# Performance work log

Measured on AMD Instinct MI355X. Metric: run time of the kernel, lower is better.

Reference implementation:

```python
import jax, jax.numpy as jnp
import numpy as np
import math

N_NODES = 20000
N_EDGES = 320000
MUL = 64          # multiplicity of each irrep block
N_BASIS = 10
N_HID = 100
W_NUMEL = 4 * MUL  # 4 'uvu' instructions, v=1


def setup_inputs() -> dict:
    key = jax.random.key(0)
    ks = jax.random.split(key, 16)
    node_input = jax.random.normal(ks[0], (N_NODES, 4 * MUL), dtype=jnp.float32)  # 64x0e + 64x1o -> 64 + 192
    node_attr = jnp.ones((N_NODES, 1), dtype=jnp.float32)
    node_deg = jax.random.randint(ks[1], (N_NODES, 1), 1, 33).astype(jnp.float32)
    edge_src = jax.random.randint(ks[2], (N_EDGES,), 0, N_NODES)
    edge_dst = jax.random.randint(ks[3], (N_EDGES,), 0, N_NODES)
    edge_attr = jax.random.normal(ks[4], (N_EDGES, 4), dtype=jnp.float32)  # sh: 1x0e + 1x1o
    edge_length_embedded = jax.random.uniform(ks[5], (N_EDGES, N_BASIS), dtype=jnp.float32)
    # FullyConnectedTensorProduct weights (node_attr is 1x0e -> per-irrep linear mixing)
    W_li0 = jax.random.normal(ks[6], (MUL, MUL), dtype=jnp.float32)
    W_li1 = jax.random.normal(ks[7], (MUL, MUL), dtype=jnp.float32)
    W_lm0 = jax.random.normal(ks[8], (MUL, MUL), dtype=jnp.float32)
    W_lm1 = jax.random.normal(ks[9], (MUL, MUL), dtype=jnp.float32)
    # radial MLP: number_of_basis -> radial_neurons -> weight_numel (no bias, e3nn FullyConnectedNet style)
    W_mlp1 = jax.random.normal(ks[10], (N_BASIS, N_HID), dtype=jnp.float32)
    W_mlp2 = jax.random.normal(ks[11], (N_HID, W_NUMEL), dtype=jnp.float32)
    # linear_output: irreps_mid (128x0e + 128x1o) x 1x0e -> 64x0e + 64x1o
    W_lo0 = jax.random.normal(ks[12], (2 * MUL, MUL), dtype=jnp.float32)
    W_lo1 = jax.random.normal(ks[13], (2 * MUL, MUL), dtype=jnp.float32)
    return dict(node_input=node_input, node_attr=node_attr, node_deg=node_deg,
                edge_attr=edge_attr, edge_length_embedded=edge_length_embedded,
                W_li0=W_li0, W_li1=W_li1, W_lm0=W_lm0, W_lm1=W_lm1,
                W_mlp1=W_mlp1, W_mlp2=W_mlp2, W_lo0=W_lo0, W_lo1=W_lo1,
                edge_src=edge_src, edge_dst=edge_dst)


def _split(x):
    # split 64x0e + 64x1o feature vector into scalar [*,64] and vector [*,64,3] parts
    s = x[..., :MUL]
    v = x[..., MUL:].reshape(x.shape[:-1] + (MUL, 3))
    return s, v


def _fctp(s, v, W0, W1, attr, fan_in):
    # FullyConnectedTensorProduct with 1x0e attr: per-irrep linear, path-normalized
    inv = 1.0 / math.sqrt(fan_in)
    o0 = jnp.einsum('nu,uk->nk', s, W0) * attr * inv
    o1 = jnp.einsum('num,uk->nkm', v, W1) * attr[..., None] * inv
    return o0, o1


def reference(node_input, node_attr, node_deg, edge_attr, edge_length_embedded,
              W_li0, W_li1, W_lm0, W_lm1, W_mlp1, W_mlp2, W_lo0, W_lo1,
              edge_src, edge_dst):
    N = node_input.shape[0]
    x0, x1 = _split(node_input)

    # linear_input then degree pre-normalization
    f0, f1 = _fctp(x0, x1, W_li0, W_li1, node_attr, MUL)
    deg_isqrt = 1.0 / jnp.sqrt(node_deg)            # [N,1]
    f0 = f0 * deg_isqrt
    f1 = f1 * deg_isqrt[..., None]

    # linear_mask (skip path)
    m0, m1 = _fctp(x0, x1, W_lm0, W_lm1, node_attr, MUL)

    # radial MLP -> per-edge tensor-product weights [E, 256]
    h = jax.nn.silu(edge_length_embedded @ W_mlp1 / math.sqrt(N_BASIS))
    ew = (h @ W_mlp2) / math.sqrt(N_HID)
    wa, wb, wc, wd = ew[:, :MUL], ew[:, MUL:2*MUL], ew[:, 2*MUL:3*MUL], ew[:, 3*MUL:]

    # gather source-node features per edge
    g0 = f0[edge_src]                                # [E,64]
    g1 = f1[edge_src]                                # [E,64,3]
    y0 = edge_attr[:, 0]                             # [E]   1x0e
    y1 = edge_attr[:, 1:4]                           # [E,3] 1x1o

    # 'uvu' tensor product paths (block-diagonal equivariant contractions)
    m0a = wa * g0 * y0[:, None]                                        # 0e x 0e -> 0e
    m0b = wb * jnp.einsum('eum,em->eu', g1, y1) / math.sqrt(3.0)       # 1o x 1o -> 0e
    m1a = wc[:, :, None] * g0[:, :, None] * y1[:, None, :]             # 0e x 1o -> 1o
    m1b = wd[:, :, None] * g1 * y0[:, None, None]                      # 1o x 0e -> 1o

    # scatter-sum into destination nodes (irreps_mid = 128x0e + 128x1o)
    s_mid = jax.ops.segment_sum(jnp.concatenate([m0a, m0b], axis=1), edge_dst, num_segments=N)          # [N,128]
    v_mid = jax.ops.segment_sum(jnp.concatenate([m1a, m1b], axis=1), edge_dst, num_segments=N)          # [N,128,3]

    # degree post-normalization
    s_mid = s_mid * deg_isqrt
    v_mid = v_mid * deg_isqrt[..., None]

    # linear_output
    o0, o1 = _fctp(s_mid, v_mid, W_lo0, W_lo1, node_attr, 2 * MUL)

    # masked skip combination; output_mask is all ones here (every out irrep is reachable)
    c_s, c_x = math.sin(math.pi / 8), math.cos(math.pi / 8)
    out0 = c_s * m0 + c_x * o0                       # [N,64]
    out1 = c_s * m1 + c_x * o1                       # [N,64,3]
    return jnp.concatenate([out0, out1.reshape(N, 3 * MUL)], axis=1)  # [N,256]
```

## Files before the change

### kernel.cpp

```cpp
#include <hip/hip_runtime.h>
#include <hip/hip_bf16.h>
#include <math.h>

#define N_NODES 20000
#define N_EDGES 320000

#define INV1   0.31622776601683794f
#define SC2    0.1f
#define IS3    0.5773502691896258f
#define C_S    0.3826834323650898f
#define C_X    0.9238795325112867f
#define INV64  0.125f
#define INVLO  0.08838834764831845f

typedef short     short8 __attribute__((ext_vector_type(8)));
typedef float     f32x4  __attribute__((ext_vector_type(4)));

__device__ __forceinline__ float silu_f(float x) {
    return x / (1.0f + expf(-x));
}
__device__ __forceinline__ unsigned short f2bf(float x) {
    __hip_bfloat16 h = __float2bfloat16(x);
    return *reinterpret_cast<unsigned short*>(&h);
}
__device__ __forceinline__ float bf2f(unsigned short u) {
    __hip_bfloat16 h;
    *reinterpret_cast<unsigned short*>(&h) = u;
    return __bfloat162float(h);
}

__global__ __launch_bounds__(256) void k_node_in(
    const float* __restrict__ ni, const float* __restrict__ attr,
    const float* __restrict__ deg,
    const float* __restrict__ Wli0, const float* __restrict__ Wli1,
    const float* __restrict__ Wlm0, const float* __restrict__ Wlm1,
    ushort4* __restrict__ fvb, float* __restrict__ out)
{
    __shared__ float raw[4][256];
    const int wave = threadIdx.x >> 6;
    const int lane = threadIdx.x & 63;
    const int n = blockIdx.x * 4 + wave;

    const float* row = ni + (size_t)n * 256;
    raw[wave][lane      ] = row[lane      ];
    raw[wave][lane + 64 ] = row[lane + 64 ];
    raw[wave][lane + 128] = row[lane + 128];
    raw[wave][lane + 192] = row[lane + 192];
    __syncthreads();

    float f0 = 0.f, m0 = 0.f;
    float f1x = 0.f, f1y = 0.f, f1z = 0.f;
    float m1x = 0.f, m1y = 0.f, m1z = 0.f;
    #pragma unroll 4
    for (int t = 0; t < 64; ++t) {
        float xs  = raw[wave][t];
        float xv0 = raw[wave][64 + t*3    ];
        float xv1 = raw[wave][64 + t*3 + 1];
        float xv2 = raw[wave][64 + t*3 + 2];
        float a0 = Wli0[t*64 + lane];
        float a1 = Wli1[t*64 + lane];
        float b0 = Wlm0[t*64 + lane];
        float b1 = Wlm1[t*64 + lane];
        f0  += xs  * a0;   m0  += xs  * b0;
        f1x += xv0 * a1;   f1y += xv1 * a1;   f1z += xv2 * a1;
        m1x += xv0 * b1;   m1y += xv1 * b1;   m1z += xv2 * b1;
    }

    const float a   = attr[n] * INV64;
    const float dis = 1.0f / sqrtf(deg[n]);
    const float fa  = a * dis;

    ushort4 pk;
    pk.x = f2bf(f0  * fa);
    pk.y = f2bf(f1x * fa);
    pk.z = f2bf(f1y * fa);
    pk.w = f2bf(f1z * fa);
    fvb[(size_t)n * 64 + lane] = pk;

    float* orow = out + (size_t)n * 256;
    orow[lane] = C_S * m0 * a;
    orow[64 + lane*3    ] = C_S * m1x * a;
    orow[64 + lane*3 + 1] = C_S * m1y * a;
    orow[64 + lane*3 + 2] = C_S * m1z * a;
}

__global__ __launch_bounds__(256) void k_w2t(
    const float* __restrict__ W2, const float* __restrict__ W1,
    unsigned short* __restrict__ w2t, unsigned short* __restrict__ w1t)
{
    const int i = blockIdx.x * 256 + threadIdx.x;
    if (i < 32768) {
        const int n = i >> 7, k = i & 127;
        w2t[i] = (k < 100) ? f2bf(W2[k*256 + n] * SC2) : (unsigned short)0;
    } else if (i < 32768 + 3584) {
        const int j = i - 32768;
        const int n = j >> 5, k = j & 31;
        w1t[j] = (k < 10 && n < 100) ? f2bf(W1[k*100 + n] * INV1)
                                     : (unsigned short)0;
    }
}

__global__ __launch_bounds__(256) void k_hist(const int* __restrict__ edst,
                                              int* __restrict__ hist) {
    const int e = blockIdx.x * 256 + threadIdx.x;
    if (e < N_EDGES) atomicAdd(&hist[edst[e]], 1);
}

__global__ __launch_bounds__(1024) void k_scan(const int* __restrict__ hist,
                                               int* __restrict__ starts,
                                               int* __restrict__ cursor) {
    __shared__ int part[1024];
    const int t = threadIdx.x;
    const int C = 20;
    const int base = t * C;
    int s = 0;
    for (int i = 0; i < C; ++i) {
        const int idx = base + i;
        if (idx < N_NODES) s += hist[idx];
    }
    part[t] = s;
    __syncthreads();
    for (int off = 1; off < 1024; off <<= 1) {
        int v = (t >= off) ? part[t - off] : 0;
        __syncthreads();
        part[t] += v;
        __syncthreads();
    }
    int run = part[t] - s;
    for (int i = 0; i < C; ++i) {
        const int idx = base + i;
        if (idx < N_NODES) {
            starts[idx] = run;
            cursor[idx] = run;
            run += hist[idx];
        }
    }
    if (t == 1023) starts[N_NODES] = N_EDGES;
}

__global__ __launch_bounds__(256) void k_scatter(
    const int* __restrict__ esrc, const int* __restrict__ edst,
    const float4* __restrict__ eattr4, const float* __restrict__ elen,
    int* __restrict__ cursor, int* __restrict__ esrc_s,
    float4* __restrict__ eattrs, unsigned short* __restrict__ elen_sb)
{
    const int e = blockIdx.x * 256 + threadIdx.x;
    if (e < N_EDGES) {
        const int p = atomicAdd(&cursor[edst[e]], 1);
        esrc_s[p] = esrc[e];
        eattrs[p] = eattr4[e];
        const float* el = elen + (size_t)e * 10;
        unsigned short v[32];
        #pragma unroll
        for (int b = 0; b < 10; ++b) v[b] = f2bf(el[b]);
        #pragma unroll
        for (int b = 10; b < 32; ++b) v[b] = 0;
        short8* dst = (short8*)(elen_sb + (size_t)p * 32);
        #pragma unroll
        for (int s = 0; s < 4; ++s) {
            short8 pk;
            #pragma unroll
            for (int j = 0; j < 8; ++j) pk[j] = (short)v[s*8 + j];
            dst[s] = pk;
        }
    }
}

__global__ __launch_bounds__(256, 4) void k_mlp(
    const unsigned short* __restrict__ elen_sb,
    const unsigned short* __restrict__ w1t,
    const unsigned short* __restrict__ w2t,
    unsigned short* __restrict__ ew)
{
    __shared__ unsigned short Hs[128 * 136];
    const int t    = threadIdx.x;
    const int w    = t >> 6;
    const int lane = t & 63;
    const int m15  = lane & 15;
    const int q    = lane >> 4;
    const int eb   = w * 32;
    const int e0   = blockIdx.x * 128;

    {
        const int r = eb + (lane >> 1);
        const int c = 112 + (lane & 1) * 8;
        short8 z = {0,0,0,0,0,0,0,0};
        *(short8*)&Hs[r*136 + c] = z;
    }

    short8 xa0 = *(const short8*)(elen_sb + (size_t)(e0 + eb      + m15)*32 + q*8);
    short8 xa1 = *(const short8*)(elen_sb + (size_t)(e0 + eb + 16 + m15)*32 + q*8);

    for (int nt = 0; nt < 7; ++nt) {
        short8 bw = *(const short8*)(w1t + (nt*16 + m15)*32 + q*8);
        f32x4 z4 = {0.f, 0.f, 0.f, 0.f};
        f32x4 h0 = __builtin_amdgcn_mfma_f32_16x16x32_bf16(xa0, bw, z4, 0, 0, 0);
        f32x4 h1 = __builtin_amdgcn_mfma_f32_16x16x32_bf16(xa1, bw, z4, 0, 0, 0);
        #pragma unroll
        for (int r = 0; r < 4; ++r) {
            Hs[(eb      + q*4 + r)*136 + nt*16 + m15] = f2bf(silu_f(h0[r]));
            Hs[(eb + 16 + q*4 + r)*136 + nt*16 + m15] = f2bf(silu_f(h1[r]));
        }
    }

    short8 A0[4], A1[4];
    #pragma unroll
    for (int s = 0; s < 4; ++s) {
        A0[s] = *(const short8*)&Hs[(eb      + m15)*136 + s*32 + q*8];
        A1[s] = *(const short8*)&Hs[(eb + 16 + m15)*136 + s*32 + q*8];
    }

    unsigned short* stg = &Hs[eb * 136];
    unsigned short* gb2 = ew + (size_t)(e0 + eb) * 256;
    #pragma unroll
    for (int half = 0; half < 2; ++half) {
        for (int nt8 = 0; nt8 < 8; ++nt8) {
            const int nt = half*8 + nt8;
            f32x4 c0 = {0.f,0.f,0.f,0.f}, c1 = {0.f,0.f,0.f,0.f};
            const unsigned short* bp = w2t + ((size_t)(nt*16 + m15) << 7);
            #pragma unroll
            for (int s = 0; s < 4; ++s) {
                short8 B = *(const short8*)(bp + s*32 + q*8);
                c0 = __builtin_amdgcn_mfma_f32_16x16x32_bf16(A0[s], B, c0, 0, 0, 0);
                c1 = __builtin_amdgcn_mfma_f32_16x16x32_bf16(A1[s], B, c1, 0, 0, 0);
            }
            #pragma unroll
            for (int r = 0; r < 4; ++r) {
                stg[(     q*4 + r)*136 + nt8*16 + m15] = f2bf(c0[r]);
                stg[(16 + q*4 + r)*136 + nt8*16 + m15] = f2bf(c1[r]);
            }
        }
        for (int r = 0; r < 32; ++r) {
            const unsigned int v =
                (unsigned int)stg[r*136 + lane] |
                ((unsigned int)stg[r*136 + 64 + lane] << 16);
            *(unsigned int*)(gb2 + (size_t)r*256 + lane*4 + half*2) = v;
        }
    }
}

__global__ __launch_bounds__(256) void k_gather(
    const int* __restrict__ starts, const int* __restrict__ esrc_s,
    const float4* __restrict__ eattrs, const unsigned short* __restrict__ ew,
    const ushort4* __restrict__ fvb,
    const float* __restrict__ attr, const float* __restrict__ deg,
    const float* __restrict__ Wlo0, const float* __restrict__ Wlo1,
    float* __restrict__ out)
{
    __shared__ float sm[4][512];
    const int wave = threadIdx.x >> 6;
    const int lane = threadIdx.x & 63;
    const int n = blockIdx.x * 4 + wave;

    const int beg = starts[n], end = starts[n + 1];
    float sA=0.f, sB=0.f;
    float vA0=0.f, vA1=0.f, vA2=0.f;
    float vB0=0.f, vB1=0.f, vB2=0.f;

    for (int base = beg; base < end; base += 64) {
        const int cnt = min(64, end - base);
        int    srcv = 0;
        float4 eav  = make_float4(0.f, 0.f, 0.f, 0.f);
        if (lane < cnt) {
            srcv = esrc_s[base + lane];
            eav  = eattrs[base + lane];
        }
        #pragma unroll 2
        for (int j = 0; j < cnt; ++j) {
            const int   src = __shfl(srcv, j);
            const float y0  = __shfl(eav.x, j);
            const float y10 = __shfl(eav.y, j);
            const float y11 = __shfl(eav.z, j);
            const float y12 = __shfl(eav.w, j);

            const ushort4 w4 = *(const ushort4*)(ew + (size_t)(base + j)*256 + lane*4);
            const float wa = bf2f(w4.x);
            const float wb = bf2f(w4.y);
            const float wc = bf2f(w4.z);
            const float wd = bf2f(w4.w);

            const ushort4 g4 = fvb[(size_t)src * 64 + lane];
            const float g0  = bf2f(g4.x);
            const float g10 = bf2f(g4.y);
            const float g11 = bf2f(g4.z);
            const float g12 = bf2f(g4.w);

            const float dotv = g10*y10 + g11*y11 + g12*y12;
            sA += wa * g0 * y0;
            sB += wb * dotv;
            const float t0 = wc * g0;
            vA0 += t0 * y10;  vA1 += t0 * y11;  vA2 += t0 * y12;
            const float t1 = wd * y0;
            vB0 += t1 * g10;  vB1 += t1 * g11;  vB2 += t1 * g12;
        }
    }

    const float dis = 1.0f / sqrtf(deg[n]);
    sm[wave][lane            ] = sA * dis;
    sm[wave][64  + lane      ] = sB * IS3 * dis;
    sm[wave][128 + lane      ] = vA0 * dis;
    sm[wave][128 + 64 + lane ] = vB0 * dis;
    sm[wave][256 + lane      ] = vA1 * dis;
    sm[wave][256 + 64 + lane ] = vB1 * dis;
    sm[wave][384 + lane      ] = vA2 * dis;
    sm[wave][384 + 64 + lane ] = vB2 * dis;
    __syncthreads();

    float o0=0.f, o1x=0.f, o1y=0.f, o1z=0.f;
    #pragma unroll 4
    for (int c = 0; c < 128; ++c) {
        const float w0 = Wlo0[c*64 + lane];
        const float w1 = Wlo1[c*64 + lane];
        o0  += sm[wave][c]         * w0;
        o1x += sm[wave][128 + c]   * w1;
        o1y += sm[wave][256 + c]   * w1;
        o1z += sm[wave][384 + c]   * w1;
    }

    const float a = attr[n] * INVLO;
    float* orow = out + (size_t)n * 256;
    orow[lane] += C_X * o0 * a;
    orow[64 + lane*3    ] += C_X * o1x * a;
    orow[64 + lane*3 + 1] += C_X * o1y * a;
    orow[64 + lane*3 + 2] += C_X * o1z * a;
}

__global__ __launch_bounds__(256) void k_node_in_legacy(
    const float* __restrict__ ni, const float* __restrict__ attr,
    const float* __restrict__ deg,
    const float* __restrict__ Wli0, const float* __restrict__ Wli1,
    const float* __restrict__ Wlm0, const float* __restrict__ Wlm1,
    float* __restrict__ f, float* __restrict__ out)
{
    __shared__ float raw[4][256];
    const int wave = threadIdx.x >> 6;
    const int lane = threadIdx.x & 63;
    const int n = blockIdx.x * 4 + wave;

    const float* row = ni + (size_t)n * 256;
    raw[wave][lane      ] = row[lane      ];
    raw[wave][lane + 64 ] = row[lane + 64 ];
    raw[wave][lane + 128] = row[lane + 128];
    raw[wave][lane + 192] = row[lane + 192];
    __syncthreads();

    float f0 = 0.f, m0 = 0.f;
    float f1x = 0.f, f1y = 0.f, f1z = 0.f;
    float m1x = 0.f, m1y = 0.f, m1z = 0.f;
    for (int t = 0; t < 64; ++t) {
        float xs  = raw[wave][t];
        float xv0 = raw[wave][64 + t*3    ];
        float xv1 = raw[wave][64 + t*3 + 1];
        float xv2 = raw[wave][64 + t*3 + 2];
        float a0 = Wli0[t*64 + lane];
        float a1 = Wli1[t*64 + lane];
        float b0 = Wlm0[t*64 + lane];
        float b1 = Wlm1[t*64 + lane];
        f0  += xs  * a0;   m0  += xs  * b0;
        f1x += xv0 * a1;   f1y += xv1 * a1;   f1z += xv2 * a1;
        m1x += xv0 * b1;   m1y += xv1 * b1;   m1z += xv2 * b1;
    }

    const float a   = attr[n] * INV64;
    const float dis = 1.0f / sqrtf(deg[n]);
    const float fa  = a * dis;

    float* fr = f + (size_t)n * 256;
    fr[lane      ] = f0  * fa;
    fr[64  + lane] = f1x * fa;
    fr[128 + lane] = f1y * fa;
    fr[192 + lane] = f1z * fa;

    float* orow = out + (size_t)n * 256;
    orow[lane] = C_S * m0 * a;
    orow[64 + lane*3    ] = C_S * m1x * a;
    orow[64 + lane*3 + 1] = C_S * m1y * a;
    orow[64 + lane*3 + 2] = C_S * m1z * a;
}

__global__ __launch_bounds__(256) void k_edge_legacy(
    const float* __restrict__ eattr, const float* __restrict__ elen,
    const float* __restrict__ W1, const float* __restrict__ W2,
    const int* __restrict__ esrc, const int* __restrict__ edst,
    const float* __restrict__ f, float* __restrict__ acc)
{
    __shared__ float hsh[4][104];
    const int wave = threadIdx.x >> 6;
    const int lane = threadIdx.x & 63;
    const int e = blockIdx.x * 4 + wave;

    const float* el = elen + (size_t)e * 10;
    float elr[10];
    #pragma unroll
    for (int b = 0; b < 10; ++b) elr[b] = el[b];

    float a1 = 0.f;
    #pragma unroll
    for (int b = 0; b < 10; ++b) a1 += elr[b] * W1[b*100 + lane];
    hsh[wave][lane] = silu_f(a1 * INV1);
    if (lane < 36) {
        float a2 = 0.f;
        #pragma unroll
        for (int b = 0; b < 10; ++b) a2 += elr[b] * W1[b*100 + 64 + lane];
        hsh[wave][64 + lane] = silu_f(a2 * INV1);
    }
    __syncthreads();

    float wa = 0.f, wb = 0.f, wc = 0.f, wd = 0.f;
    for (int j = 0; j < 100; ++j) {
        float hj = hsh[wave][j];
        const float* wr = W2 + j*256;
        wa += hj * wr[lane      ];
        wb += hj * wr[64  + lane];
        wc += hj * wr[128 + lane];
        wd += hj * wr[192 + lane];
    }
    wa *= SC2; wb *= SC2; wc *= SC2; wd *= SC2;

    const int src = esrc[e];
    const int dst = edst[e];
    const float y0  = eattr[e*4 + 0];
    const float y10 = eattr[e*4 + 1];
    const float y11 = eattr[e*4 + 2];
    const float y12 = eattr[e*4 + 3];

    const float* fr = f + (size_t)src * 256;
    const float g0  = fr[lane      ];
    const float g10 = fr[64  + lane];
    const float g11 = fr[128 + lane];
    const float g12 = fr[192 + lane];

    const float dotv = g10*y10 + g11*y11 + g12*y12;

    float* ar = acc + (size_t)dst * 512;
    atomicAdd(ar + lane,                  wa * g0 * y0);
    atomicAdd(ar + 64 + lane,             wb * dotv * IS3);
    atomicAdd(ar + 128 +   0 + lane,      wc * g0 * y10);
    atomicAdd(ar + 128 + 128 + lane,      wc * g0 * y11);
    atomicAdd(ar + 128 + 256 + lane,      wc * g0 * y12);
    atomicAdd(ar + 128 +   0 + 64 + lane, wd * g10 * y0);
    atomicAdd(ar + 128 + 128 + 64 + lane, wd * g11 * y0);
    atomicAdd(ar + 128 + 256 + 64 + lane, wd * g12 * y0);
}

__global__ __launch_bounds__(256) void k_node_out_legacy(
    const float* __restrict__ acc, const float* __restrict__ attr,
    const float* __restrict__ deg, const float* __restrict__ Wlo0,
    const float* __restrict__ Wlo1, float* __restrict__ out)
{
    __shared__ float sm[4][512];
    const int wave = threadIdx.x >> 6;
    const int lane = threadIdx.x & 63;
    const int n = blockIdx.x * 4 + wave;

    const float dis = 1.0f / sqrtf(deg[n]);
    const float* ar = acc + (size_t)n * 512;
    for (int i = lane; i < 512; i += 64) sm[wave][i] = ar[i] * dis;
    __syncthreads();

    float o0 = 0.f, o1x = 0.f, o1y = 0.f, o1z = 0.f;
    for (int c = 0; c < 128; ++c) {
        float w0 = Wlo0[c*64 + lane];
        float w1 = Wlo1[c*64 + lane];
        o0  += sm[wave][c]        * w0;
        o1x += sm[wave][128 + c]  * w1;
        o1y += sm[wave][256 + c]  * w1;
        o1z += sm[wave][384 + c]  * w1;
    }

    const float a = attr[n] * INVLO;
    float* orow = out + (size_t)n * 256;
    orow[lane] += C_X * o0 * a;
    orow[64 + lane*3    ] += C_X * o1x * a;
    orow[64 + lane*3 + 1] += C_X * o1y * a;
    orow[64 + lane*3 + 2] += C_X * o1z * a;
}

extern "C" void kernel_launch(void* const* d_in, const int* in_sizes, int n_in,
                              void* d_out, int out_size, void* d_ws, size_t ws_size,
                              hipStream_t stream) {
    const float* ni    = (const float*)d_in[0];
    const float* attr  = (const float*)d_in[1];
    const float* deg   = (const float*)d_in[2];
    const float* eattr = (const float*)d_in[3];
    const float* elen  = (const float*)d_in[4];
    const float* Wli0  = (const float*)d_in[5];
    const float* Wli1  = (const float*)d_in[6];
    const float* Wlm0  = (const float*)d_in[7];
    const float* Wlm1  = (const float*)d_in[8];
    const float* Wm1   = (const float*)d_in[9];
    const float* Wm2   = (const float*)d_in[10];
    const float* Wlo0  = (const float*)d_in[11];
    const float* Wlo1  = (const float*)d_in[12];
    const int*   esrc  = (const int*)d_in[13];
    const int*   edst  = (const int*)d_in[14];

    float* out = (float*)d_out;

    char* wsb = (char*)d_ws;
    size_t off = 0;
    ushort4* fvb = (ushort4*)(wsb + off);               off += (size_t)N_NODES * 64 * 8;
    unsigned short* ew = (unsigned short*)(wsb + off);  off += (size_t)N_EDGES * 256 * 2;
    unsigned short* elen_sb = (unsigned short*)(wsb + off); off += (size_t)N_EDGES * 32 * 2;
    float4* eattrs = (float4*)(wsb + off);              off += (size_t)N_EDGES * 16;
    int* esrc_s = (int*)(wsb + off);                    off += (size_t)N_EDGES * 4;
    unsigned short* w2t = (unsigned short*)(wsb + off); off += 32768 * 2;
    unsigned short* w1t = (unsigned short*)(wsb + off); off += 3584 * 2;
    int* starts = (int*)(wsb + off);                    off += (size_t)(N_NODES + 4) * 4;
    int* hist   = (int*)(wsb + off);                    off += (size_t)N_NODES * 4;
    int* cursor = (int*)(wsb + off);                    off += (size_t)N_NODES * 4;
    const size_t need_fast = off;

    if (ws_size >= need_fast) {
        hipMemsetAsync(hist, 0, (size_t)N_NODES * sizeof(int), stream);
        k_node_in<<<N_NODES / 4, 256, 0, stream>>>(ni, attr, deg, Wli0, Wli1,
                                                   Wlm0, Wlm1, fvb, out);
        k_w2t    <<<144, 256, 0, stream>>>(Wm2, Wm1, w2t, w1t);
        k_hist   <<<N_EDGES / 256, 256, 0, stream>>>(edst, hist);
        k_scan   <<<1, 1024, 0, stream>>>(hist, starts, cursor);
        k_scatter<<<N_EDGES / 256, 256, 0, stream>>>(esrc, edst,
                                                     (const float4*)eattr, elen,
                                                     cursor, esrc_s, eattrs, elen_sb);
        k_mlp    <<<N_EDGES / 128, 256, 0, stream>>>(elen_sb, w1t, w2t, ew);
        k_gather <<<N_NODES / 4, 256, 0, stream>>>(starts, esrc_s, eattrs, ew,
                                                   fvb, attr, deg, Wlo0, Wlo1, out);
    } else {
        float* f   = (float*)d_ws;
        float* acc = f + (size_t)N_NODES * 256;
        hipMemsetAsync(acc, 0, (size_t)N_NODES * 512 * sizeof(float), stream);
        k_node_in_legacy<<<N_NODES / 4, 256, 0, stream>>>(ni, attr, deg, Wli0, Wli1,
                                                          Wlm0, Wlm1, f, out);
        k_edge_legacy<<<N_EDGES / 4, 256, 0, stream>>>(eattr, elen, Wm1, Wm2,
                                                       esrc, edst, f, acc);
        k_node_out_legacy<<<N_NODES / 4, 256, 0, stream>>>(acc, attr, deg,
                                                           Wlo0, Wlo1, out);
    }
}
```

Measured before the change: 414.8 us.

## Batch gather loads eight edges deep and split output linear into separate kernel

New measurement: 451.4 us. 8.8% more time.

```diff
diff --git a/kernel.cpp b/kernel.cpp
--- a/kernel.cpp
+++ b/kernel.cpp
@@ -239,15 +239,11 @@
     }
 }
 
-__global__ __launch_bounds__(256) void k_gather(
+__global__ __launch_bounds__(256) void k_gather2(
     const int* __restrict__ starts, const int* __restrict__ esrc_s,
     const float4* __restrict__ eattrs, const unsigned short* __restrict__ ew,
-    const ushort4* __restrict__ fvb,
-    const float* __restrict__ attr, const float* __restrict__ deg,
-    const float* __restrict__ Wlo0, const float* __restrict__ Wlo1,
-    float* __restrict__ out)
-{
-    __shared__ float sm[4][512];
+    const ushort4* __restrict__ fvb, ushort4* __restrict__ acc)
+{
     const int wave = threadIdx.x >> 6;
     const int lane = threadIdx.x & 63;
     const int n = blockIdx.x * 4 + wave;
@@ -265,56 +261,88 @@
             srcv = esrc_s[base + lane];
             eav  = eattrs[base + lane];
         }
-        #pragma unroll 2
-        for (int j = 0; j < cnt; ++j) {
-            const int   src = __shfl(srcv, j);
-            const float y0  = __shfl(eav.x, j);
-            const float y10 = __shfl(eav.y, j);
-            const float y11 = __shfl(eav.z, j);
-            const float y12 = __shfl(eav.w, j);
-
-            const ushort4 w4 = *(const ushort4*)(ew + (size_t)(base + j)*256 + lane*4);
-            const float wa = bf2f(w4.x);
-            const float wb = bf2f(w4.y);
-            const float wc = bf2f(w4.z);
-            const float wd = bf2f(w4.w);
-
-            const ushort4 g4 = fvb[(size_t)src * 64 + lane];
-            const float g0  = bf2f(g4.x);
-            const float g10 = bf2f(g4.y);
-            const float g11 = bf2f(g4.z);
-            const float g12 = bf2f(g4.w);
-
-            const float dotv = g10*y10 + g11*y11 + g12*y12;
-            sA += wa * g0 * y0;
-            sB += wb * dotv;
-            const float t0 = wc * g0;
-            vA0 += t0 * y10;  vA1 += t0 * y11;  vA2 += t0 * y12;
-            const float t1 = wd * y0;
-            vB0 += t1 * g10;  vB1 += t1 * g11;  vB2 += t1 * g12;
-        }
-    }
+        for (int j0 = 0; j0 < cnt; j0 += 8) {
+            const int m = min(8, cnt - j0);
+            ushort4 wv[8], gv[8];
+            #pragma unroll
+            for (int i = 0; i < 8; ++i) {
+                if (i < m) {
+                    const int src = __shfl(srcv, j0 + i);
+                    wv[i] = *(const ushort4*)(ew + (size_t)(base + j0 + i)*256 + lane*4);
+                    gv[i] = fvb[(size_t)src * 64 + lane];
+                }
+            }
+            #pragma unroll
+            for (int i = 0; i < 8; ++i) {
+                if (i < m) {
+                    const float y0  = __shfl(eav.x, j0 + i);
+                    const float y10 = __shfl(eav.y, j0 + i);
+                    const float y11 = __shfl(eav.z, j0 + i);
+                    const float y12 = __shfl(eav.w, j0 + i);
+
+                    const float wa = bf2f(wv[i].x);
+                    const float wb = bf2f(wv[i].y);
+                    const float wc = bf2f(wv[i].z);
+                    const float wd = bf2f(wv[i].w);
+
+                    const float g0  = bf2f(gv[i].x);
+                    const float g10 = bf2f(gv[i].y);
+                    const float g11 = bf2f(gv[i].z);
+                    const float g12 = bf2f(gv[i].w);
+
+                    const float dotv = g10*y10 + g11*y11 + g12*y12;
+                    sA += wa * g0 * y0;
+                    sB += wb * dotv;
+                    const float t0 = wc * g0;
+                    vA0 += t0 * y10;  vA1 += t0 * y11;  vA2 += t0 * y12;
+                    const float t1 = wd * y0;
+                    vB0 += t1 * g10;  vB1 += t1 * g11;  vB2 += t1 * g12;
+                }
+            }
+        }
+    }
+
+    ushort4 p0, p1;
+    p0.x = f2bf(sA);        p0.y = f2bf(sB * IS3);
+    p0.z = f2bf(vA0);       p0.w = f2bf(vB0);
+    p1.x = f2bf(vA1);       p1.y = f2bf(vB1);
+    p1.z = f2bf(vA2);       p1.w = f2bf(vB2);
+    acc[(size_t)n * 128 + lane]      = p0;
+    acc[(size_t)n * 128 + 64 + lane] = p1;
+}
+
+__global__ __launch_bounds__(256) void k_node_out(
+    const ushort4* __restrict__ acc, const float* __restrict__ attr,
+    const float* __restrict__ deg, const float* __restrict__ Wlo0,
+    const float* __restrict__ Wlo1, float* __restrict__ out)
+{
+    __shared__ float sm[4][512];
+    const int wave = threadIdx.x >> 6;
+    const int lane = threadIdx.x & 63;
+    const int n = blockIdx.x * 4 + wave;
 
     const float dis = 1.0f / sqrtf(deg[n]);
-    sm[wave][lane            ] = sA * dis;
-    sm[wave][64  + lane      ] = sB * IS3 * dis;
-    sm[wave][128 + lane      ] = vA0 * dis;
-    sm[wave][128 + 64 + lane ] = vB0 * dis;
-    sm[wave][256 + lane      ] = vA1 * dis;
-    sm[wave][256 + 64 + lane ] = vB1 * dis;
-    sm[wave][384 + lane      ] = vA2 * dis;
-    sm[wave][384 + 64 + lane ] = vB2 * dis;
+    const ushort4 p0 = acc[(size_t)n * 128 + lane];
+    const ushort4 p1 = acc[(size_t)n * 128 + 64 + lane];
+    sm[wave][lane      ] = bf2f(p0.x) * dis;
+    sm[wave][64  + lane] = bf2f(p0.y) * dis;
+    sm[wave][128 + lane] = bf2f(p0.z) * dis;
+    sm[wave][192 + lane] = bf2f(p0.w) * dis;
+    sm[wave][256 + lane] = bf2f(p1.x) * dis;
+    sm[wave][320 + lane] = bf2f(p1.y) * dis;
+    sm[wave][384 + lane] = bf2f(p1.z) * dis;
+    sm[wave][448 + lane] = bf2f(p1.w) * dis;
     __syncthreads();
 
-    float o0=0.f, o1x=0.f, o1y=0.f, o1z=0.f;
+    float o0 = 0.f, o1x = 0.f, o1y = 0.f, o1z = 0.f;
     #pragma unroll 4
     for (int c = 0; c < 128; ++c) {
         const float w0 = Wlo0[c*64 + lane];
         const float w1 = Wlo1[c*64 + lane];
-        o0  += sm[wave][c]         * w0;
-        o1x += sm[wave][128 + c]   * w1;
-        o1y += sm[wave][256 + c]   * w1;
-        o1z += sm[wave][384 + c]   * w1;
+        o0  += sm[wave][c]        * w0;
+        o1x += sm[wave][128 + c]  * w1;
+        o1y += sm[wave][256 + c]  * w1;
+        o1z += sm[wave][384 + c]  * w1;
     }
 
     const float a = attr[n] * INVLO;
@@ -511,6 +539,8 @@
     int* cursor = (int*)(wsb + off);                    off += (size_t)N_NODES * 4;
     const size_t need_fast = off;
 
+    ushort4* acc = (ushort4*)elen_sb;
+
     if (ws_size >= need_fast) {
         hipMemsetAsync(hist, 0, (size_t)N_NODES * sizeof(int), stream);
         k_node_in<<<N_NODES / 4, 256, 0, stream>>>(ni, attr, deg, Wli0, Wli1,
@@ -522,17 +552,18 @@
                                                      (const float4*)eattr, elen,
                                                      cursor, esrc_s, eattrs, elen_sb);
         k_mlp    <<<N_EDGES / 128, 256, 0, stream>>>(elen_sb, w1t, w2t, ew);
-        k_gather <<<N_NODES / 4, 256, 0, stream>>>(starts, esrc_s, eattrs, ew,
-                                                   fvb, attr, deg, Wlo0, Wlo1, out);
+        k_gather2<<<N_NODES / 4, 256, 0, stream>>>(starts, esrc_s, eattrs, ew,
+                                                   fvb, acc);
+        k_node_out<<<N_NODES / 4, 256, 0, stream>>>(acc, attr, deg, Wlo0, Wlo1, out);
     } else {
         float* f   = (float*)d_ws;
-        float* acc = f + (size_t)N_NODES * 256;
-        hipMemsetAsync(acc, 0, (size_t)N_NODES * 512 * sizeof(float), stream);
+        float* accf = f + (size_t)N_NODES * 256;
+        hipMemsetAsync(accf, 0, (size_t)N_NODES * 512 * sizeof(float), stream);
         k_node_in_legacy<<<N_NODES / 4, 256, 0, stream>>>(ni, attr, deg, Wli0, Wli1,
                                                           Wlm0, Wlm1, f, out);
         k_edge_legacy<<<N_EDGES / 4, 256, 0, stream>>>(eattr, elen, Wm1, Wm2,
-                                                       esrc, edst, f, acc);
-        k_node_out_legacy<<<N_NODES / 4, 256, 0, stream>>>(acc, attr, deg,
+                                                       esrc, edst, f, accf);
+        k_node_out_legacy<<<N_NODES / 4, 256, 0, stream>>>(accf, attr, deg,
                                                            Wlo0, Wlo1, out);
     }
 }
```
